# Performance work log

Hardware: AMD Instinct MI355X
Metric: run time of the kernel (lower is better)

## Reference

```python
import jax, jax.numpy as jnp
import numpy as np

B, T, C, H = 256, 256, 384, 64
MAX_REL = 3  # max_relative_position hardcoded in module


def setup_inputs() -> dict:
    key = jax.random.key(0)
    ks = jax.random.split(key, 6)
    s = 1.0 / np.sqrt(C)
    return {
        "x": jax.random.normal(ks[0], (B, T, C), dtype=jnp.float32),
        "Wq": jax.random.normal(ks[1], (C, H), dtype=jnp.float32) * s,
        "Wk": jax.random.normal(ks[2], (C, H), dtype=jnp.float32) * s,
        "Wv": jax.random.normal(ks[3], (C, H), dtype=jnp.float32) * s,
        "rel_k_table": jax.random.normal(ks[4], (2 * MAX_REL + 1, H), dtype=jnp.float32) * s,
        "rel_v_table": jax.random.normal(ks[5], (2 * MAX_REL + 1, H), dtype=jnp.float32) * s,
    }


def reference(x, Wq, Wk, Wv, rel_k_table, rel_v_table):
    Bd, Td, Cd = x.shape
    Hd = Wq.shape[1]
    q = x @ Wq  # [B,T,H]
    k = x @ Wk
    v = x @ Wv
    # relative position indices, clipped Shaw-style
    r = jnp.arange(Td)
    idx = jnp.clip(r[None, :] - r[:, None], -MAX_REL, MAX_REL) + MAX_REL  # [T,T]
    rk = rel_k_table[idx]  # [T,T,H]
    rv = rel_v_table[idx]  # [T,T,H]
    attn1 = jnp.einsum('bth,bsh->bts', q, k)
    attn2 = jnp.einsum('bth,tsh->bts', q, rk)
    scale = jnp.sqrt(jnp.asarray(Hd, dtype=x.dtype))
    scores = (attn1 + attn2) / scale
    causal = jnp.tril(jnp.ones((Td, Td), dtype=bool))
    scores = jnp.where(causal[None, :, :], scores, -jnp.inf)
    attn = jax.nn.softmax(scores, axis=-1)  # dropout = identity (eval mode)
    w1 = jnp.einsum('bts,bsh->bth', attn, v)
    w2 = jnp.einsum('bts,tsh->bth', attn, rv)
    return w1 + w2  # [B,T,H]
```

## Files before the change

kernel.cpp:

```cpp
#include <hip/hip_runtime.h>
#include <hip/hip_bf16.h>


typedef __attribute__((ext_vector_type(8))) __bf16 bf16x8;
typedef __attribute__((ext_vector_type(8))) short short8;
typedef __attribute__((ext_vector_type(4))) float f32x4;
typedef __attribute__((ext_vector_type(4))) int   i32x4;

#define MFMA16(A, B, C) __builtin_amdgcn_mfma_f32_16x16x32_bf16((A), (B), (C), 0, 0, 0)

__device__ __forceinline__ unsigned short f2bf(float f) {
    unsigned int u = __builtin_bit_cast(unsigned int, f);
    u = (u + 0x7FFFu + ((u >> 16) & 1u)) >> 16;
    return (unsigned short)u;
}
__device__ __forceinline__ float bf2f(unsigned short s) {
    unsigned int u = ((unsigned int)s) << 16;
    return __builtin_bit_cast(float, u);
}
__device__ __forceinline__ bf16x8 ld16(const unsigned short* p) {
    return __builtin_bit_cast(bf16x8, *(const i32x4*)p);
}

__global__ void prep_wt(const float* __restrict__ Wq, const float* __restrict__ Wk,
                        const float* __restrict__ Wv, const float* __restrict__ relk,
                        unsigned short* __restrict__ Wt, unsigned short* __restrict__ Rk) {
    int i = blockIdx.x * 256 + threadIdx.x;
    if (i < 3 * 64 * 384) {
        int kk = i % 384;
        int h  = (i / 384) & 63;
        int w  = i / (384 * 64);
        const float* W = (w == 0) ? Wq : ((w == 1) ? Wk : Wv);
        Wt[i] = f2bf(W[kk * 64 + h]);
    } else if (i < 3 * 64 * 384 + 1024) {
        int j = i - 3 * 64 * 384;
        int n = j >> 6, h = j & 63;
        Rk[j] = (n < 4) ? f2bf(relk[n * 64 + h]) : (unsigned short)0;
    }
}

__global__ __launch_bounds__(512) void qkv_kernel(
        const float* __restrict__ x, const unsigned short* __restrict__ Wt,
        unsigned short* __restrict__ q, unsigned short* __restrict__ k,
        unsigned short* __restrict__ vT) {
    __shared__ unsigned short wlds[192][136];

    const int tid  = threadIdx.x;
    const int wave = tid >> 6;
    const int lane = tid & 63;
    const int c    = lane & 15;
    const int quad = lane >> 4;
    const int M0   = blockIdx.x * 128;
    const int myrow = M0 + wave * 16 + c;

    f32x4 zero = {0.f, 0.f, 0.f, 0.f};
    f32x4 aq[4], ak[4], av[4];
#pragma unroll
    for (int i = 0; i < 4; i++) { aq[i] = zero; ak[i] = zero; av[i] = zero; }

    for (int ck = 0; ck < 3; ck++) {
        if (ck) __syncthreads();
#pragma unroll
        for (int it = 0; it < 6; it++) {
            int i = it * 512 + tid;
            int r = i >> 4, kc = i & 15;
            i32x4 d = *(const i32x4*)(Wt + r * 384 + ck * 128 + kc * 8);
            *(i32x4*)(&wlds[r][kc * 8]) = d;
        }
        __syncthreads();

#pragma unroll
        for (int ks = 0; ks < 4; ks++) {
            const float* xp = x + (size_t)myrow * 384 + ck * 128 + ks * 32 + quad * 8;
            f32x4 x0 = *(const f32x4*)xp;
            f32x4 x1 = *(const f32x4*)(xp + 4);
            short8 xs;
#pragma unroll
            for (int j = 0; j < 4; j++) {
                xs[j]     = (short)f2bf(x0[j]);
                xs[4 + j] = (short)f2bf(x1[j]);
            }
            bf16x8 a = __builtin_bit_cast(bf16x8, xs);

#pragma unroll
            for (int nt = 0; nt < 8; nt++) {
                bf16x8 b = ld16(&wlds[nt * 16 + c][ks * 32 + quad * 8]);
                if (nt < 4) aq[nt]     = MFMA16(a, b, aq[nt]);
                else        ak[nt - 4] = MFMA16(a, b, ak[nt - 4]);
            }
#pragma unroll
            for (int mt = 0; mt < 4; mt++) {
                bf16x8 aw = ld16(&wlds[128 + mt * 16 + c][ks * 32 + quad * 8]);
                av[mt] = MFMA16(aw, a, av[mt]);
            }
        }
    }

    const int b   = M0 >> 8;
    const int t0b = M0 & 255;
#pragma unroll
    for (int nt = 0; nt < 4; nt++) {
#pragma unroll
        for (int r = 0; r < 4; r++) {
            int row = M0 + wave * 16 + quad * 4 + r;
            q[row * 64 + nt * 16 + c] = f2bf(aq[nt][r]);
            k[row * 64 + nt * 16 + c] = f2bf(ak[nt][r]);
        }
    }
#pragma unroll
    for (int mt = 0; mt < 4; mt++) {
#pragma unroll
        for (int r = 0; r < 4; r++) {
            int h = mt * 16 + quad * 4 + r;
            vT[(b * 64 + h) * 256 + t0b + wave * 16 + c] = f2bf(av[mt][r]);
        }
    }
}

__global__ __launch_bounds__(64, 4) void attn_kernel(
        const unsigned short* __restrict__ q, const unsigned short* __restrict__ k,
        const unsigned short* __restrict__ vT, const unsigned short* __restrict__ Rk,
        const float* __restrict__ relv, float* __restrict__ out) {
    __shared__ unsigned short P[16][264];
    __shared__ float E[16][4];

    const int lane = threadIdx.x;
    const int c    = lane & 15;
    const int quad = lane >> 4;
    const int tt   = blockIdx.x;
    const int b    = blockIdx.y;
    const int t0   = tt * 16;
    const int nst  = tt + 1;

    f32x4 zero = {0.f, 0.f, 0.f, 0.f};

    float rv[4][4];
#pragma unroll
    for (int j = 0; j < 4; j++)
#pragma unroll
        for (int nt = 0; nt < 4; nt++) rv[j][nt] = relv[j * 64 + nt * 16 + c];

    const unsigned short* qp = q + (size_t)(b * 256 + t0 + c) * 64 + quad * 8;
    bf16x8 aq0 = ld16(qp);
    bf16x8 aq1 = ld16(qp + 32);

    {
        f32x4 e = zero;
        e = MFMA16(aq0, ld16(Rk + c * 64 + quad * 8), e);
        e = MFMA16(aq1, ld16(Rk + c * 64 + 32 + quad * 8), e);
        if (c < 4) {
#pragma unroll
            for (int r = 0; r < 4; r++) E[quad * 4 + r][c] = e[r];
        }
    }
    __syncthreads();
    f32x4 ef[4];
#pragma unroll
    for (int r = 0; r < 4; r++) ef[r] = *(const f32x4*)(&E[quad * 4 + r][0]);

    float l[4] = {0.f, 0.f, 0.f, 0.f};
#pragma unroll
    for (int st = 0; st < 16; st++) {
        if (st < nst) {
            const unsigned short* kp = k + (size_t)(b * 256 + st * 16 + c) * 64 + quad * 8;
            f32x4 s = zero;
            s = MFMA16(aq0, ld16(kp), s);
            s = MFMA16(aq1, ld16(kp + 32), s);
#pragma unroll
            for (int r = 0; r < 4; r++) {
                int tg = t0 + quad * 4 + r;
                int sg = st * 16 + c;
                int d  = sg - tg;
                float e = (d <= -3) ? ef[r][0] : (d == -2) ? ef[r][1]
                        : (d == -1) ? ef[r][2] : ef[r][3];
                float p = (d > 0) ? 0.f : __expf(0.125f * (s[r] + e));
                l[r] += p;
                P[quad * 4 + r][sg] = f2bf(p);
            }
        }
    }
    if (nst & 1) {
#pragma unroll
        for (int r = 0; r < 4; r++) P[quad * 4 + r][nst * 16 + c] = 0;
    }
#pragma unroll
    for (int r = 0; r < 4; r++)
#pragma unroll
        for (int ofs = 1; ofs < 16; ofs <<= 1)
            l[r] += __shfl_xor(l[r], ofs, 64);
    float rl[4];
#pragma unroll
    for (int r = 0; r < 4; r++) rl[r] = 1.0f / l[r];
    __syncthreads();

    f32x4 o[4];
#pragma unroll
    for (int nt = 0; nt < 4; nt++) o[nt] = zero;
    const int ksteps = (nst + 1) >> 1;
#pragma unroll
    for (int ks = 0; ks < 8; ks++) {
        if (ks < ksteps) {
            bf16x8 ap = ld16(&P[c][ks * 32 + quad * 8]);
#pragma unroll
            for (int nt = 0; nt < 4; nt++) {
                const unsigned short* vp = vT + (size_t)(b * 64 + nt * 16 + c) * 256
                                              + ks * 32 + quad * 8;
                o[nt] = MFMA16(ap, ld16(vp), o[nt]);
            }
        }
    }

#pragma unroll
    for (int r = 0; r < 4; r++) {
        int tl = quad * 4 + r;
        int tg = t0 + tl;
        float pa = (tg >= 2) ? bf2f(P[tl][tg - 2]) * rl[r] : 0.f;
        float pb = (tg >= 1) ? bf2f(P[tl][tg - 1]) * rl[r] : 0.f;
        float pc = bf2f(P[tl][tg]) * rl[r];
#pragma unroll
        for (int nt = 0; nt < 4; nt++) {
            float r0 = rv[0][nt];
            float w2 = r0 + pa * (rv[1][nt] - r0) + pb * (rv[2][nt] - r0)
                          + pc * (rv[3][nt] - r0);
            out[(size_t)(b * 256 + tg) * 64 + nt * 16 + c] = o[nt][r] * rl[r] + w2;
        }
    }
}

extern "C" void kernel_launch(void* const* d_in, const int* in_sizes, int n_in,
                              void* d_out, int out_size, void* d_ws, size_t ws_size,
                              hipStream_t stream) {
    const float* x    = (const float*)d_in[0];
    const float* Wq   = (const float*)d_in[1];
    const float* Wk   = (const float*)d_in[2];
    const float* Wv   = (const float*)d_in[3];
    const float* relk = (const float*)d_in[4];
    const float* relv = (const float*)d_in[5];
    float* out = (float*)d_out;

    char* ws = (char*)d_ws;
    unsigned short* q  = (unsigned short*)(ws);
    unsigned short* kk = (unsigned short*)(ws + 8388608);
    unsigned short* vT = (unsigned short*)(ws + 16777216);
    unsigned short* Wt = (unsigned short*)(ws + 25165824);
    unsigned short* Rk = (unsigned short*)(ws + 25313280);

    prep_wt<<<292, 256, 0, stream>>>(Wq, Wk, Wv, relk, Wt, Rk);
    qkv_kernel<<<512, 512, 0, stream>>>(x, Wt, q, kk, vT);
    attn_kernel<<<dim3(16, 256), 64, 0, stream>>>(q, kk, vT, Rk, relv, out);
}
```

Before: 208.5 us.

## Stage full weight matrix in LDS and software-prefetch x, K, V tiles

The QKV kernel now loads all three transposed weight matrices into 150KB of dynamic LDS in one pass instead of three chunked passes with barriers. It also double-buffers the x row loads in registers so the next chunk is fetched while MFMAs run on the current one. The attention kernel turns the unrolled masked loops over K and V tiles into runtime-bounded loops that prefetch the next tile into registers. The large LDS footprint limits the QKV kernel to one block per CU and raises register pressure.

```diff
diff --git a/kernel.cpp b/kernel.cpp
--- a/kernel.cpp
+++ b/kernel.cpp
@@ -39,86 +39,94 @@
     }
 }
 
-__global__ __launch_bounds__(512) void qkv_kernel(
+__global__ __launch_bounds__(512, 1) void qkv_kernel(
         const float* __restrict__ x, const unsigned short* __restrict__ Wt,
         unsigned short* __restrict__ q, unsigned short* __restrict__ k,
         unsigned short* __restrict__ vT) {
-    __shared__ unsigned short wlds[192][136];
+    extern __shared__ unsigned short ws[];
 
     const int tid  = threadIdx.x;
     const int wave = tid >> 6;
     const int lane = tid & 63;
     const int c    = lane & 15;
     const int quad = lane >> 4;
-    const int M0   = blockIdx.x * 128;
-    const int myrow = M0 + wave * 16 + c;
+    const int row0 = blockIdx.x * 128;
+    const int myrow = row0 + wave * 16 + c;
+
+    const float* xp0 = x + (size_t)myrow * 384;
+
+    f32x4 xb[2][8];
+#pragma unroll
+    for (int j = 0; j < 4; j++) {
+        xb[0][2 * j]     = *(const f32x4*)(xp0 + j * 32 + quad * 8);
+        xb[0][2 * j + 1] = *(const f32x4*)(xp0 + j * 32 + quad * 8 + 4);
+    }
+
+#pragma unroll
+    for (int it = 0; it < 18; it++) {
+        int P = it * 512 + tid;
+        int r = P / 48, pc = P % 48;
+        i32x4 d = *(const i32x4*)(Wt + r * 384 + pc * 8);
+        *(i32x4*)(ws + r * 392 + pc * 8) = d;
+    }
+    __syncthreads();
 
     f32x4 zero = {0.f, 0.f, 0.f, 0.f};
     f32x4 aq[4], ak[4], av[4];
 #pragma unroll
     for (int i = 0; i < 4; i++) { aq[i] = zero; ak[i] = zero; av[i] = zero; }
 
+#pragma unroll
     for (int ck = 0; ck < 3; ck++) {
-        if (ck) __syncthreads();
-#pragma unroll
-        for (int it = 0; it < 6; it++) {
-            int i = it * 512 + tid;
-            int r = i >> 4, kc = i & 15;
-            i32x4 d = *(const i32x4*)(Wt + r * 384 + ck * 128 + kc * 8);
-            *(i32x4*)(&wlds[r][kc * 8]) = d;
-        }
-        __syncthreads();
-
-#pragma unroll
-        for (int ks = 0; ks < 4; ks++) {
-            const float* xp = x + (size_t)myrow * 384 + ck * 128 + ks * 32 + quad * 8;
-            f32x4 x0 = *(const f32x4*)xp;
-            f32x4 x1 = *(const f32x4*)(xp + 4);
-            short8 xs;
+        const int cur = ck & 1;
+        if (ck < 2) {
 #pragma unroll
             for (int j = 0; j < 4; j++) {
-                xs[j]     = (short)f2bf(x0[j]);
-                xs[4 + j] = (short)f2bf(x1[j]);
+                const float* xp = xp0 + (ck + 1) * 128 + j * 32 + quad * 8;
+                xb[1 - cur][2 * j]     = *(const f32x4*)xp;
+                xb[1 - cur][2 * j + 1] = *(const f32x4*)(xp + 4);
             }
-            bf16x8 a = __builtin_bit_cast(bf16x8, xs);
-
-#pragma unroll
-            for (int nt = 0; nt < 8; nt++) {
-                bf16x8 b = ld16(&wlds[nt * 16 + c][ks * 32 + quad * 8]);
-                if (nt < 4) aq[nt]     = MFMA16(a, b, aq[nt]);
-                else        ak[nt - 4] = MFMA16(a, b, ak[nt - 4]);
+        }
+#pragma unroll
+        for (int j = 0; j < 4; j++) {
+            short8 xs8;
+#pragma unroll
+            for (int e = 0; e < 4; e++) {
+                xs8[e]     = (short)f2bf(xb[cur][2 * j][e]);
+                xs8[4 + e] = (short)f2bf(xb[cur][2 * j + 1][e]);
             }
-#pragma unroll
-            for (int mt = 0; mt < 4; mt++) {
-                bf16x8 aw = ld16(&wlds[128 + mt * 16 + c][ks * 32 + quad * 8]);
-                av[mt] = MFMA16(aw, a, av[mt]);
+            bf16x8 a = __builtin_bit_cast(bf16x8, xs8);
+            const int col = (ck * 4 + j) * 32 + quad * 8;
+
+#pragma unroll
+            for (int nt = 0; nt < 4; nt++) {
+                bf16x8 bq = ld16(ws + (nt * 16 + c) * 392 + col);
+                bf16x8 bk = ld16(ws + (64 + nt * 16 + c) * 392 + col);
+                bf16x8 aw = ld16(ws + (128 + nt * 16 + c) * 392 + col);
+                aq[nt] = MFMA16(a, bq, aq[nt]);
+                ak[nt] = MFMA16(a, bk, ak[nt]);
+                av[nt] = MFMA16(aw, a, av[nt]);
             }
         }
     }
 
-    const int b   = M0 >> 8;
-    const int t0b = M0 & 255;
+    const int b   = row0 >> 8;
+    const int t0b = row0 & 255;
 #pragma unroll
     for (int nt = 0; nt < 4; nt++) {
 #pragma unroll
         for (int r = 0; r < 4; r++) {
-            int row = M0 + wave * 16 + quad * 4 + r;
+            int row = row0 + wave * 16 + quad * 4 + r;
             q[row * 64 + nt * 16 + c] = f2bf(aq[nt][r]);
             k[row * 64 + nt * 16 + c] = f2bf(ak[nt][r]);
-        }
-    }
-#pragma unroll
-    for (int mt = 0; mt < 4; mt++) {
-#pragma unroll
-        for (int r = 0; r < 4; r++) {
-            int h = mt * 16 + quad * 4 + r;
-            vT[(b * 64 + h) * 256 + t0b + wave * 16 + c] = f2bf(av[mt][r]);
+            int h = nt * 16 + quad * 4 + r;
+            vT[(b * 64 + h) * 256 + t0b + wave * 16 + c] = f2bf(av[nt][r]);
         }
     }
 }
 
 __global__ __launch_bounds__(64, 4) void attn_kernel(
-        const unsigned short* __restrict__ q, const unsigned short* __restrict__ k,
+        const unsigned short* __restrict__ q, const unsigned short* __restrict__ kg,
         const unsigned short* __restrict__ vT, const unsigned short* __restrict__ Rk,
         const float* __restrict__ relv, float* __restrict__ out) {
     __shared__ unsigned short P[16][264];
@@ -134,12 +142,6 @@
 
     f32x4 zero = {0.f, 0.f, 0.f, 0.f};
 
-    float rv[4][4];
-#pragma unroll
-    for (int j = 0; j < 4; j++)
-#pragma unroll
-        for (int nt = 0; nt < 4; nt++) rv[j][nt] = relv[j * 64 + nt * 16 + c];
-
     const unsigned short* qp = q + (size_t)(b * 256 + t0 + c) * 64 + quad * 8;
     bf16x8 aq0 = ld16(qp);
     bf16x8 aq1 = ld16(qp + 32);
@@ -158,26 +160,37 @@
 #pragma unroll
     for (int r = 0; r < 4; r++) ef[r] = *(const f32x4*)(&E[quad * 4 + r][0]);
 
+    float rv[4][4];
+#pragma unroll
+    for (int j = 0; j < 4; j++)
+#pragma unroll
+        for (int nt = 0; nt < 4; nt++) rv[j][nt] = relv[j * 64 + nt * 16 + c];
+
+    const unsigned short* kbase = kg + (size_t)b * 256 * 64;
     float l[4] = {0.f, 0.f, 0.f, 0.f};
-#pragma unroll
-    for (int st = 0; st < 16; st++) {
-        if (st < nst) {
-            const unsigned short* kp = k + (size_t)(b * 256 + st * 16 + c) * 64 + quad * 8;
-            f32x4 s = zero;
-            s = MFMA16(aq0, ld16(kp), s);
-            s = MFMA16(aq1, ld16(kp + 32), s);
-#pragma unroll
-            for (int r = 0; r < 4; r++) {
-                int tg = t0 + quad * 4 + r;
-                int sg = st * 16 + c;
-                int d  = sg - tg;
-                float e = (d <= -3) ? ef[r][0] : (d == -2) ? ef[r][1]
-                        : (d == -1) ? ef[r][2] : ef[r][3];
-                float p = (d > 0) ? 0.f : __expf(0.125f * (s[r] + e));
-                l[r] += p;
-                P[quad * 4 + r][sg] = f2bf(p);
-            }
-        }
+    bf16x8 ka = ld16(kbase + (size_t)c * 64 + quad * 8);
+    bf16x8 kb2 = ld16(kbase + (size_t)c * 64 + 32 + quad * 8);
+    for (int st = 0; st < nst; st++) {
+        bf16x8 na = ka, nb = kb2;
+        if (st + 1 < nst) {
+            const unsigned short* kp = kbase + (size_t)((st + 1) * 16 + c) * 64 + quad * 8;
+            na = ld16(kp);
+            nb = ld16(kp + 32);
+        }
+        f32x4 s = MFMA16(aq0, ka, zero);
+        s = MFMA16(aq1, kb2, s);
+        int R = st * 16 + c;
+#pragma unroll
+        for (int r = 0; r < 4; r++) {
+            int tg = t0 + quad * 4 + r;
+            int d  = R - tg;
+            float ee = (d <= -3) ? ef[r][0] : (d == -2) ? ef[r][1]
+                     : (d == -1) ? ef[r][2] : ef[r][3];
+            float p = (d > 0) ? 0.f : __expf(0.125f * (s[r] + ee));
+            l[r] += p;
+            P[quad * 4 + r][R] = f2bf(p);
+        }
+        ka = na; kb2 = nb;
     }
     if (nst & 1) {
 #pragma unroll
@@ -193,21 +206,29 @@
     for (int r = 0; r < 4; r++) rl[r] = 1.0f / l[r];
     __syncthreads();
 
+    const unsigned short* vbase = vT + (size_t)b * 64 * 256;
     f32x4 o[4];
 #pragma unroll
     for (int nt = 0; nt < 4; nt++) o[nt] = zero;
     const int ksteps = (nst + 1) >> 1;
-#pragma unroll
-    for (int ks = 0; ks < 8; ks++) {
-        if (ks < ksteps) {
-            bf16x8 ap = ld16(&P[c][ks * 32 + quad * 8]);
-#pragma unroll
-            for (int nt = 0; nt < 4; nt++) {
-                const unsigned short* vp = vT + (size_t)(b * 64 + nt * 16 + c) * 256
-                                              + ks * 32 + quad * 8;
-                o[nt] = MFMA16(ap, ld16(vp), o[nt]);
-            }
-        }
+    bf16x8 vf[4];
+#pragma unroll
+    for (int nt = 0; nt < 4; nt++)
+        vf[nt] = ld16(vbase + (size_t)(nt * 16 + c) * 256 + quad * 8);
+    for (int ks = 0; ks < ksteps; ks++) {
+        bf16x8 nv[4];
+#pragma unroll
+        for (int nt = 0; nt < 4; nt++) nv[nt] = vf[nt];
+        if (ks + 1 < ksteps) {
+#pragma unroll
+            for (int nt = 0; nt < 4; nt++)
+                nv[nt] = ld16(vbase + (size_t)(nt * 16 + c) * 256 + (ks + 1) * 32 + quad * 8);
+        }
+        bf16x8 ap = ld16(&P[c][ks * 32 + quad * 8]);
+#pragma unroll
+        for (int nt = 0; nt < 4; nt++) o[nt] = MFMA16(ap, vf[nt], o[nt]);
+#pragma unroll
+        for (int nt = 0; nt < 4; nt++) vf[nt] = nv[nt];
     }
 
 #pragma unroll
@@ -245,7 +266,10 @@
     unsigned short* Wt = (unsigned short*)(ws + 25165824);
     unsigned short* Rk = (unsigned short*)(ws + 25313280);
 
+    (void)hipFuncSetAttribute((const void*)qkv_kernel,
+                              hipFuncAttributeMaxDynamicSharedMemorySize, 150528);
+
     prep_wt<<<292, 256, 0, stream>>>(Wq, Wk, Wv, relk, Wt, Rk);
-    qkv_kernel<<<512, 512, 0, stream>>>(x, Wt, q, kk, vT);
+    qkv_kernel<<<512, 512, 150528, stream>>>(x, Wt, q, kk, vT);
     attn_kernel<<<dim3(16, 256), 64, 0, stream>>>(q, kk, vT, Rk, relv, out);
 }
```

New measurement: 205.0 us. Within noise of the previous version (-1.7%).
